# Kernel optimization log

Measured on AMD Instinct MI355X. Metric: run time of the kernel, lower is better.

Reference implementation:

```python
import jax, jax.numpy as jnp
import numpy as np

# Module constants from CheckboxDetector.__init__ / _postprocess
N = 8192            # candidate detections
C = 2               # checkbox classes (checked / unchecked)
THR = 0.7           # confidence threshold (self.threshold)
IOU_THR = 0.5       # torchvision.ops.nms iou_threshold
INPUT_H, INPUT_W = 1280.0, 1280.0   # self.input_shape
IMG_H, IMG_W = 2480.0, 3508.0       # original image (A4 @ 300dpi)
SCALER = max(IMG_W / INPUT_W, IMG_H / INPUT_H)
EPS = 1e-9


def setup_inputs() -> dict:
    key = jax.random.key(0)
    k1, k2, k3 = jax.random.split(key, 3)
    cls_conf = jax.random.uniform(k1, (N, C), dtype=jnp.float32)
    # well-formed xyxy boxes inside the 1280x1280 canvas
    xy = jax.random.uniform(k2, (N, 2), dtype=jnp.float32, minval=0.0, maxval=1200.0)
    wh = jax.random.uniform(k3, (N, 2), dtype=jnp.float32, minval=8.0, maxval=80.0)
    bboxes = jnp.concatenate([xy, xy + wh], axis=1)  # [N,4]
    return {"cls_conf": cls_conf, "bboxes": bboxes}


def _pairwise_iou(boxes):
    # boxes: [N,4] xyxy -> iou: [N,N]
    x1, y1, x2, y2 = boxes[:, 0], boxes[:, 1], boxes[:, 2], boxes[:, 3]
    area = (x2 - x1) * (y2 - y1)
    iw = jnp.clip(jnp.minimum(x2[:, None], x2[None, :]) - jnp.maximum(x1[:, None], x1[None, :]), 0.0)
    ih = jnp.clip(jnp.minimum(y2[:, None], y2[None, :]) - jnp.maximum(y1[:, None], y1[None, :]), 0.0)
    inter = iw * ih
    return inter / (area[:, None] + area[None, :] - inter + EPS)


def reference(cls_conf, bboxes):
    # _threshold: keep rows with any class confidence > THR (mask instead of
    # dynamic filtering, for fixed shapes under jit)
    valid = jnp.any(cls_conf > THR, axis=1)            # [N]
    scores = jnp.max(cls_conf, axis=1)                 # cls_conf.max(1)
    masked_scores = jnp.where(valid, scores, -jnp.inf)

    # _nms: sort by score desc, greedy IoU suppression (torchvision semantics)
    order = jnp.argsort(-masked_scores)
    b = bboxes[order]          # [N,4]
    c = cls_conf[order]        # [N,C]
    v = valid[order]           # [N]

    iou = _pairwise_iou(b)     # [N,N]  (256 MB: memory-bound core)
    idx = jnp.arange(N)

    def body(i, keep):
        # box i (if still kept & valid) suppresses later boxes overlapping > IOU_THR
        sup = (iou[i] > IOU_THR) & (idx > i) & keep[i]
        return keep & ~sup

    keep = jax.lax.fori_loop(0, N, body, v)            # [N] bool

    # _postprocess tail: rescale boxes to original image size; suppressed
    # detections are zeroed (mask semantics in place of dynamic gather).
    kf = keep.astype(cls_conf.dtype)[:, None]
    boxes_out = b * SCALER * kf                        # [N,4]
    conf_out = c * kf                                  # [N,C]
    return jnp.concatenate([boxes_out, conf_out], axis=1)  # [N, 4+C]
```

## Files before the change

### kernel.cpp

```cpp
#include <hip/hip_runtime.h>
#include <math.h>

#define N_BOX 8192
#define NW 128
#define NTHR 512
#define LCAP 24576
#define NRBLK 128
#define NPTILE 576
#define WPB 8
#define NWAVE (NPTILE * WPB)
#define SLOT 128
#define WSPT (NWAVE / NTHR)
#define NCH 8
#define THR_C 0.7f
#define IOU_THR_C 0.5f
#define EPS_C 1e-9f

__device__ __constant__ float kScaler = (float)(3508.0 / 1280.0);

static __device__ __forceinline__ unsigned long long key_from(float c0, float c1, int i) {
    bool valid = (c0 > THR_C) || (c1 > THR_C);
    float ms = valid ? fmaxf(c0, c1) : -INFINITY;
    unsigned int u = __float_as_uint(ms);
    unsigned int m = (u & 0x80000000u) ? ~u : (u | 0x80000000u);
    unsigned int d = ~m;
    return ((unsigned long long)d << 32) | (unsigned int)i;
}

__global__ __launch_bounds__(NTHR) void stageA(const float* __restrict__ conf,
                                               const float* __restrict__ bboxes,
                                               int* __restrict__ partial,
                                               unsigned long long* __restrict__ validw,
                                               unsigned int* __restrict__ wcnt,
                                               unsigned int* __restrict__ wslot) {
    int b = blockIdx.x;
    int t = threadIdx.x;
    int lane = t & 63;
    if (b < NRBLK) {
        __align__(16) __shared__ unsigned long long ck[1024];
        __shared__ unsigned long long rk[512];
        __shared__ int nvcS, nvrS;
        int ech = b >> 3;
        int cch = b & 7;
        if (t == 0) { nvcS = 0; nvrS = 0; }
        __syncthreads();
        for (int l = t; l < 1024; l += NTHR) {
            int j = (cch << 10) + l;
            float2 cc = ((const float2*)conf)[j];
            bool v = (cc.x > THR_C) || (cc.y > THR_C);
            unsigned long long bal = __ballot(v);
            int cnt = __popcll(bal);
            int base = 0;
            if (lane == 0 && cnt) base = atomicAdd(&nvcS, cnt);
            base = __shfl(base, 0, 64);
            if (v) ck[base + __popcll(bal & ((1ull << lane) - 1ull))] =
                       key_from(cc.x, cc.y, j);
        }
        {
            int i = (ech << 9) + t;
            float2 ci = ((const float2*)conf)[i];
            bool iv = (ci.x > THR_C) || (ci.y > THR_C);
            unsigned long long bal = __ballot(iv);
            if (cch == 0 && lane == 0) validw[i >> 6] = bal;
            int cnt = __popcll(bal);
            int base = 0;
            if (lane == 0 && cnt) base = atomicAdd(&nvrS, cnt);
            base = __shfl(base, 0, 64);
            if (iv) rk[base + __popcll(bal & ((1ull << lane) - 1ull))] =
                        key_from(ci.x, ci.y, i);
        }
        __syncthreads();
        int nvc = nvcS, nvr = nvrS;
        if (t < nvr) {
            unsigned long long ki = rk[t];
            const ulonglong2* ckp = (const ulonglong2*)ck;
            int a0 = 0, a1 = 0, a2 = 0, a3 = 0;
            int p = 0, np = nvc >> 1;
            for (; p + 2 <= np; p += 2) {
                ulonglong2 u = ckp[p];
                ulonglong2 v = ckp[p + 1];
                a0 += (u.x < ki) ? 1 : 0;
                a1 += (u.y < ki) ? 1 : 0;
                a2 += (v.x < ki) ? 1 : 0;
                a3 += (v.y < ki) ? 1 : 0;
            }
            int cnt = (a0 + a1) + (a2 + a3);
            for (int l = p << 1; l < nvc; ++l) cnt += (ck[l] < ki) ? 1 : 0;
            int i = (int)(ki & 0xffffffffull);
            partial[i * NCH + cch] = cnt;
        }
    } else {
        int pb = b - NRBLK;
        int g = 0;
        while (8 * (g + 1) * (g + 2) <= pb) ++g;
        int off = pb - 8 * g * (g + 1);
        int wq = off / (g + 1);
        int w = (g << 4) + wq;
        int h = off - wq * (g + 1);
        int waveid = pb * WPB + (t >> 6);
        __shared__ float4 cb[64];
        __shared__ float ca02[64];
        __shared__ unsigned long long cbk[64];
        __shared__ unsigned char cjr[64];
        __shared__ unsigned long long jvS;
        __shared__ int nvjS;
        if (t < 64) {
            int j = (w << 6) + t;
            float2 cc = ((const float2*)conf)[j];
            bool v = (cc.x > THR_C) || (cc.y > THR_C);
            unsigned long long bv = __ballot(v);
            if (v) {
                int pos = __popcll(bv & ((1ull << t) - 1ull));
                float4 c = ((const float4*)bboxes)[j];
                cb[pos] = c;
                ca02[pos] = 0.2f * ((c.z - c.x) * (c.w - c.y));
                cbk[pos] = key_from(cc.x, cc.y, j);
                cjr[pos] = (unsigned char)t;
            }
            if (t == 0) { jvS = bv; nvjS = __popcll(bv); }
        }
        __syncthreads();
        unsigned long long jv = jvS;
        int nvj = nvjS;
        int ibase = h << 10;
        int i0 = ibase + t;
        int i1 = i0 + 512;
        float2 cc0 = ((const float2*)conf)[i0];
        float2 cc1 = ((const float2*)conf)[i1];
        int km0, km1;
        {
            int rel = i0 - (w << 6);
            bool iv = (cc0.x > THR_C) || (cc0.y > THR_C);
            if (!iv || rel >= 63)      km0 = 64;
            else if (rel >= 0)         km0 = __popcll(jv & ((2ull << rel) - 1ull));
            else                       km0 = 0;
        }
        {
            int rel = i1 - (w << 6);
            bool iv = (cc1.x > THR_C) || (cc1.y > THR_C);
            if (!iv || rel >= 63)      km1 = 64;
            else if (rel >= 0)         km1 = __popcll(jv & ((2ull << rel) - 1ull));
            else                       km1 = 0;
        }
        int wc = 0;
        if (__any((km0 < nvj) || (km1 < nvj))) {
            float4 rb0 = ((const float4*)bboxes)[i0];
            float4 rb1 = ((const float4*)bboxes)[i1];
            float raF0 = (rb0.z - rb0.x) * (rb0.w - rb0.y);
            float raF1 = (rb1.z - rb1.x) * (rb1.w - rb1.y);
            float raS0 = 0.2f * raF0;
            float raS1 = 0.2f * raF1;
            unsigned long long ki0 = key_from(cc0.x, cc0.y, i0);
            unsigned long long ki1 = key_from(cc1.x, cc1.y, i1);
            unsigned long long bits0 = 0ull, bits1 = 0ull;
            for (int bb = 0; bb < nvj; ++bb) {
                float4 c = cb[bb];
                float s2 = ca02[bb];
                float iw0 = fminf(rb0.z, c.z) - fmaxf(rb0.x, c.x);
                float ih0 = fminf(rb0.w, c.w) - fmaxf(rb0.y, c.y);
                float inter0 = fmaxf(iw0, 0.0f) * fmaxf(ih0, 0.0f);
                if (inter0 > raS0 + s2) {
                    float caF = (c.z - c.x) * (c.w - c.y);
                    float iou = inter0 / (raF0 + caF - inter0 + EPS_C);
                    if (iou > IOU_THR_C) bits0 |= (1ull << bb);
                }
                float iw1 = fminf(rb1.z, c.z) - fmaxf(rb1.x, c.x);
                float ih1 = fminf(rb1.w, c.w) - fmaxf(rb1.y, c.y);
                float inter1 = fmaxf(iw1, 0.0f) * fmaxf(ih1, 0.0f);
                if (inter1 > raS1 + s2) {
                    float caF = (c.z - c.x) * (c.w - c.y);
                    float iou = inter1 / (raF1 + caF - inter1 + EPS_C);
                    if (iou > IOU_THR_C) bits1 |= (1ull << bb);
                }
            }
            {
                unsigned long long m = (km0 >= 64) ? 0ull : (~0ull << km0);
                unsigned long long eb = bits0 & m;
                if (__any(eb != 0ull)) {
                    int ec = __popcll(eb);
                    int pre = ec;
#pragma unroll
                    for (int d = 1; d < 64; d <<= 1) {
                        int vv = __shfl_up(pre, d, 64);
                        if (lane >= d) pre += vv;
                    }
                    int tot = __shfl(pre, 63, 64);
                    int idx = wc + pre - ec;
                    unsigned long long tb = eb;
                    while (tb) {
                        int bb = __builtin_ctzll(tb); tb &= tb - 1;
                        if (idx < SLOT) {
                            int j = (w << 6) + (int)cjr[bb];
                            unsigned int e = (ki0 < cbk[bb])
                                             ? (((unsigned int)i0 << 13) | (unsigned int)j)
                                             : (((unsigned int)j << 13) | (unsigned int)i0);
                            wslot[(size_t)waveid * SLOT + idx] = e;
                        }
                        ++idx;
                    }
                    wc += tot;
                }
            }
            {
                unsigned long long m = (km1 >= 64) ? 0ull : (~0ull << km1);
                unsigned long long eb = bits1 & m;
                if (__any(eb != 0ull)) {
                    int ec = __popcll(eb);
                    int pre = ec;
#pragma unroll
                    for (int d = 1; d < 64; d <<= 1) {
                        int vv = __shfl_up(pre, d, 64);
                        if (lane >= d) pre += vv;
                    }
                    int tot = __shfl(pre, 63, 64);
                    int idx = wc + pre - ec;
                    unsigned long long tb = eb;
                    while (tb) {
                        int bb = __builtin_ctzll(tb); tb &= tb - 1;
                        if (idx < SLOT) {
                            int j = (w << 6) + (int)cjr[bb];
                            unsigned int e = (ki1 < cbk[bb])
                                             ? (((unsigned int)i1 << 13) | (unsigned int)j)
                                             : (((unsigned int)j << 13) | (unsigned int)i1);
                            wslot[(size_t)waveid * SLOT + idx] = e;
                        }
                        ++idx;
                    }
                    wc += tot;
                }
            }
        }
        if (lane == 0) wcnt[waveid] = (unsigned int)wc;
    }
}

__global__ __launch_bounds__(NTHR) void stageB(const float* __restrict__ conf,
                                               const float* __restrict__ bboxes,
                                               const int* __restrict__ partial,
                                               const unsigned long long* __restrict__ validw,
                                               const unsigned int* __restrict__ wcnt,
                                               const unsigned int* __restrict__ wslot,
                                               float* __restrict__ out) {
    __shared__ unsigned int eL[LCAP];
    __shared__ int sinv[N_BOX];
    __shared__ unsigned long long kL[NW], tL[NW], vL[NW];
    __shared__ int wsum[WPB];
    __shared__ int totS;
    __shared__ int chg[3];
    __shared__ int fbF, nvF;
    int t = threadIdx.x;
    int lane = t & 63;
    int wv = t >> 6;
    if (t == 0) { fbF = 0; nvF = 0; chg[0] = 0; chg[1] = 0; chg[2] = 0; }
    if (t < NW) {
        unsigned long long v = validw[t];
        vL[t] = v; kL[t] = v;
        atomicAdd(&nvF, __popcll(v));
    }
    int nq[WSPT], myo[WSPT];
    int s = 0;
    bool ov = false;
#pragma unroll
    for (int q = 0; q < WSPT; ++q) {
        int v = (int)wcnt[t * WSPT + q];
        nq[q] = v; myo[q] = s; s += v;
        if (v > SLOT) ov = true;
    }
    int pre = s;
#pragma unroll
    for (int d = 1; d < 64; d <<= 1) {
        int v = __shfl_up(pre, d, 64);
        if (lane >= d) pre += v;
    }
    if (lane == 63) wsum[wv] = pre;
    __syncthreads();
    if (t == 0) {
        int acc = 0;
#pragma unroll
        for (int q = 0; q < WPB; ++q) { int v = wsum[q]; wsum[q] = acc; acc += v; }
        totS = acc;
    }
    __syncthreads();
    int ebase = wsum[wv] + (pre - s);
    int totE = totS;
    if (ov || totE > LCAP) fbF = 1;
    {
        const int4* p4 = (const int4*)partial;
        for (int base = 0; base < N_BOX; base += NTHR) {
            int i = base + t;
            if ((vL[i >> 6] >> (i & 63)) & 1ull) {
                int4 pa = p4[i * 2];
                int4 pb2 = p4[i * 2 + 1];
                int r = ((pa.x + pa.y) + (pa.z + pa.w))
                      + ((pb2.x + pb2.y) + (pb2.z + pb2.w));
                sinv[r] = i;
            }
        }
    }
    __syncthreads();
    int fb = fbF;
    if (!fb) {
#pragma unroll
        for (int q = 0; q < WSPT; ++q) {
            int w2 = t * WSPT + q;
            int off = ebase + myo[q];
            for (int k = 0; k < nq[q]; ++k)
                eL[off + k] = wslot[(size_t)w2 * SLOT + k];
        }
    }
    __syncthreads();
    if (!fb) {
        for (int it = 0; it < N_BOX; ++it) {
            if (t < NW) tL[t] = 0ull;
            __syncthreads();
            for (int e = t; e < totE; e += NTHR) {
                unsigned int ed = eL[e];
                int src = (int)(ed >> 13);
                if ((kL[src >> 6] >> (src & 63)) & 1ull) {
                    int tg = (int)(ed & 8191u);
                    atomicOr(&tL[tg >> 6], 1ull << (tg & 63));
                }
            }
            __syncthreads();
            if (t < NW) {
                unsigned long long nk = vL[t] & ~tL[t];
                if (nk != kL[t]) chg[it % 3] = 1;
                kL[t] = nk;
            }
            if (t == 0) chg[(it + 2) % 3] = 0;
            __syncthreads();
            if (chg[it % 3] == 0) break;
        }
    } else {
        if (t < NW) { tL[t] = 0ull; kL[t] = 0ull; }
        __syncthreads();
        int nv = nvF;
        if (t < 64) {
            for (int a = 0; a < nv - 1; ++a) {
                bool rem = (tL[a >> 6] >> (a & 63)) & 1ull;
                if (!rem) {
                    float4 r = ((const float4*)bboxes)[sinv[a]];
                    float ra = (r.z - r.x) * (r.w - r.y);
                    for (int b2 = a + 1 + t; b2 < nv; b2 += 64) {
                        float4 c = ((const float4*)bboxes)[sinv[b2]];
                        float ca = (c.z - c.x) * (c.w - c.y);
                        float iw = fminf(r.z, c.z) - fmaxf(r.x, c.x);
                        float ih = fminf(r.w, c.w) - fmaxf(r.y, c.y);
                        iw = fmaxf(iw, 0.0f);
                        ih = fmaxf(ih, 0.0f);
                        float inter = iw * ih;
                        float iou = inter / (ra + ca - inter + EPS_C);
                        if (iou > IOU_THR_C) atomicOr(&tL[b2 >> 6], 1ull << (b2 & 63));
                    }
                }
            }
        }
        __syncthreads();
        for (int a = t; a < nvF; a += NTHR) {
            if (!((tL[a >> 6] >> (a & 63)) & 1ull)) {
                int ia = sinv[a];
                atomicOr(&kL[ia >> 6], 1ull << (ia & 63));
            }
        }
    }
    __syncthreads();
    int nv = nvF;
    for (int base = 0; base < N_BOX; base += NTHR) {
        int r = base + t;
        bool kept = false;
        int i = 0;
        if (r < nv) {
            i = sinv[r];
            kept = (kL[i >> 6] >> (i & 63)) & 1ull;
        }
        if (kept) {
            float4 bx = ((const float4*)bboxes)[i];
            float2 cc = ((const float2*)conf)[i];
            out[r * 6 + 0] = bx.x * kScaler;
            out[r * 6 + 1] = bx.y * kScaler;
            out[r * 6 + 2] = bx.z * kScaler;
            out[r * 6 + 3] = bx.w * kScaler;
            out[r * 6 + 4] = cc.x;
            out[r * 6 + 5] = cc.y;
        } else {
            out[r * 6 + 0] = 0.0f;
            out[r * 6 + 1] = 0.0f;
            out[r * 6 + 2] = 0.0f;
            out[r * 6 + 3] = 0.0f;
            out[r * 6 + 4] = 0.0f;
            out[r * 6 + 5] = 0.0f;
        }
    }
}

extern "C" void kernel_launch(void* const* d_in, const int* in_sizes, int n_in,
                              void* d_out, int out_size, void* d_ws, size_t ws_size,
                              hipStream_t stream) {
    const float* cls_conf = (const float*)d_in[0];
    const float* bboxes   = (const float*)d_in[1];
    float* out = (float*)d_out;

    char* ws = (char*)d_ws;
    int*                partial = (int*)(ws + 0);
    unsigned int*       wcnt    = (unsigned int*)(ws + 262144);
    unsigned long long* validw  = (unsigned long long*)(ws + 282624);
    unsigned int*       wslot   = (unsigned int*)(ws + 286720);
    (void)ws_size; (void)in_sizes; (void)n_in; (void)out_size;

    stageA<<<NRBLK + NPTILE, NTHR, 0, stream>>>(cls_conf, bboxes, partial, validw, wcnt, wslot);
    stageB<<<1, NTHR, 0, stream>>>(cls_conf, bboxes, partial, validw, wcnt, wslot, out);
}
```

Measured before the change: 95.21 us.

## Split rank counting across two threads per row and trim fixpoint loop barriers

The rank-count phase in stageA now gives each valid row two threads, each scanning half of the candidate keys, and combines the halves through shared memory. This uses more of the block's threads when few rows are valid, at the cost of an extra barrier. The fixpoint loop clears the suppression mask together with the keep update, which removes one __syncthreads per iteration. Per-wave edge counts and slots are now read with q*NTHR+t, so consecutive threads read consecutive words and the loads coalesce.

After: 94.96 us. No clear change (-0.3%).

```diff
diff --git a/kernel.cpp b/kernel.cpp
--- a/kernel.cpp
+++ b/kernel.cpp
@@ -39,6 +39,7 @@
     if (b < NRBLK) {
         __align__(16) __shared__ unsigned long long ck[1024];
         __shared__ unsigned long long rk[512];
+        __shared__ int rcnt[1024];
         __shared__ int nvcS, nvrS;
         int ech = b >> 3;
         int cch = b & 7;
@@ -71,23 +72,32 @@
         }
         __syncthreads();
         int nvc = nvcS, nvr = nvrS;
-        if (t < nvr) {
-            unsigned long long ki = rk[t];
-            const ulonglong2* ckp = (const ulonglong2*)ck;
-            int a0 = 0, a1 = 0, a2 = 0, a3 = 0;
-            int p = 0, np = nvc >> 1;
-            for (; p + 2 <= np; p += 2) {
+        int npairs = nvc >> 1;
+        int nslots = nvr << 1;
+        const ulonglong2* ckp = (const ulonglong2*)ck;
+        for (int slot = t; slot < nslots; slot += NTHR) {
+            int row = slot >> 1, half = slot & 1;
+            unsigned long long ki = rk[row];
+            int lo = half ? (npairs >> 1) : 0;
+            int hi = half ? npairs : (npairs >> 1);
+            int a0 = 0, a1 = 0;
+#pragma unroll 4
+            for (int p = lo; p < hi; ++p) {
                 ulonglong2 u = ckp[p];
-                ulonglong2 v = ckp[p + 1];
                 a0 += (u.x < ki) ? 1 : 0;
                 a1 += (u.y < ki) ? 1 : 0;
-                a2 += (v.x < ki) ? 1 : 0;
-                a3 += (v.y < ki) ? 1 : 0;
-            }
-            int cnt = (a0 + a1) + (a2 + a3);
-            for (int l = p << 1; l < nvc; ++l) cnt += (ck[l] < ki) ? 1 : 0;
+            }
+            int cnt = a0 + a1;
+            if (half) {
+                for (int l = npairs << 1; l < nvc; ++l) cnt += (ck[l] < ki) ? 1 : 0;
+            }
+            rcnt[slot] = cnt;
+        }
+        __syncthreads();
+        for (int row = t; row < nvr; row += NTHR) {
+            unsigned long long ki = rk[row];
             int i = (int)(ki & 0xffffffffull);
-            partial[i * NCH + cch] = cnt;
+            partial[i * NCH + cch] = rcnt[2 * row] + rcnt[2 * row + 1];
         }
     } else {
         int pb = b - NRBLK;
@@ -254,7 +264,7 @@
     if (t == 0) { fbF = 0; nvF = 0; chg[0] = 0; chg[1] = 0; chg[2] = 0; }
     if (t < NW) {
         unsigned long long v = validw[t];
-        vL[t] = v; kL[t] = v;
+        vL[t] = v; kL[t] = v; tL[t] = 0ull;
         atomicAdd(&nvF, __popcll(v));
     }
     int nq[WSPT], myo[WSPT];
@@ -262,7 +272,7 @@
     bool ov = false;
 #pragma unroll
     for (int q = 0; q < WSPT; ++q) {
-        int v = (int)wcnt[t * WSPT + q];
+        int v = (int)wcnt[q * NTHR + t];
         nq[q] = v; myo[q] = s; s += v;
         if (v > SLOT) ov = true;
     }
@@ -302,7 +312,7 @@
     if (!fb) {
 #pragma unroll
         for (int q = 0; q < WSPT; ++q) {
-            int w2 = t * WSPT + q;
+            int w2 = q * NTHR + t;
             int off = ebase + myo[q];
             for (int k = 0; k < nq[q]; ++k)
                 eL[off + k] = wslot[(size_t)w2 * SLOT + k];
@@ -311,8 +321,6 @@
     __syncthreads();
     if (!fb) {
         for (int it = 0; it < N_BOX; ++it) {
-            if (t < NW) tL[t] = 0ull;
-            __syncthreads();
             for (int e = t; e < totE; e += NTHR) {
                 unsigned int ed = eL[e];
                 int src = (int)(ed >> 13);
@@ -323,9 +331,11 @@
             }
             __syncthreads();
             if (t < NW) {
-                unsigned long long nk = vL[t] & ~tL[t];
+                unsigned long long tt = tL[t];
+                unsigned long long nk = vL[t] & ~tt;
                 if (nk != kL[t]) chg[it % 3] = 1;
                 kL[t] = nk;
+                tL[t] = 0ull;
             }
             if (t == 0) chg[(it + 2) % 3] = 0;
             __syncthreads();
```
